# Performance work log

Measured on AMD Instinct MI355X. Metric: run time of the kernel, lower is better.

Reference implementation:

```python
import jax, jax.numpy as jnp
import numpy as np

EMBEDDING_DIM = 64
NUM_EMBEDDINGS = 512


def setup_inputs() -> dict:
    key = jax.random.key(0)
    k1, k2 = jax.random.split(key)
    inputs = jax.random.normal(k1, (64, 32, 32, EMBEDDING_DIM), dtype=jnp.float32)
    # codebook: (embedding_dim, num_embeddings), matching the Keras weight layout
    embeddings = jax.random.normal(k2, (EMBEDDING_DIM, NUM_EMBEDDINGS), dtype=jnp.float32)
    return {"inputs": inputs, "embeddings": embeddings}


def reference(inputs, embeddings):
    input_shape = inputs.shape
    flat = inputs.reshape(-1, EMBEDDING_DIM)  # [N, D]
    distances = (
        jnp.sum(flat * flat, axis=1, keepdims=True)
        + jnp.sum(embeddings * embeddings, axis=0, keepdims=True)
        - 2.0 * (flat @ embeddings)
    )  # [N, K]
    encoding_indices = jnp.argmin(distances, axis=1)  # [N]
    # one-hot @ embeddings.T == row gather from embeddings.T
    quantized = jnp.take(embeddings.T, encoding_indices, axis=0)  # [N, D]
    quantized = quantized.reshape(input_shape)
    return quantized, encoding_indices
```

## Files before the change

### kernel.cpp

```cpp
#include <hip/hip_runtime.h>

#define D 64
#define K 512
#define NT (K / 16)
#define TAU 0.01f

typedef float  f32x4  __attribute__((ext_vector_type(4)));
typedef short  bf16x8 __attribute__((ext_vector_type(8)));

__device__ inline unsigned short bf16_rne(float f) {
    union { float f; unsigned u; } v; v.f = f;
    unsigned r = v.u + 0x7FFFu + ((v.u >> 16) & 1u);
    return (unsigned short)(r >> 16);
}
__device__ inline float bf16_val(unsigned short b) {
    union { float f; unsigned u; } v; v.u = ((unsigned)b) << 16;
    return v.f;
}
__device__ inline void split8(const float* p, bf16x8& h, bf16x8& l) {
    float4 a = *(const float4*)p;
    float4 b = *(const float4*)(p + 4);
    float f[8] = {a.x, a.y, a.z, a.w, b.x, b.y, b.z, b.w};
#pragma unroll
    for (int j = 0; j < 8; ++j) {
        unsigned short hb = bf16_rne(f[j]);
        float lo = f[j] - bf16_val(hb);
        h[j] = (short)hb;
        l[j] = (short)bf16_rne(lo);
    }
}

__global__ void vq_prep(const float* __restrict__ emb,
                        float* __restrict__ embT,
                        float* __restrict__ enorm,
                        bf16x8* __restrict__ bhi,
                        bf16x8* __restrict__ blo) {
    int t = blockIdx.x * blockDim.x + threadIdx.x;
    int nt = t >> 7, c = (t >> 6) & 1, lane = t & 63;
    int k  = nt * 16 + (lane & 15);
    int d0 = c * 32 + ((lane >> 4) << 3);
    bf16x8 h, l;
#pragma unroll
    for (int j = 0; j < 8; ++j) {
        float xv = emb[(d0 + j) * K + k];
        unsigned short hb = bf16_rne(xv);
        float lo = xv - bf16_val(hb);
        h[j] = (short)hb;
        l[j] = (short)bf16_rne(lo);
    }
    int off = (nt * 2 + c) * 64 + lane;
    bhi[off] = h; blo[off] = l;

    if (t < K) {
        float s = 0.f;
#pragma unroll
        for (int d = 0; d < D; ++d) {
            float v = emb[d * K + t];
            embT[t * D + d] = v;
            s += v * v;
        }
        enorm[t] = s;
    }
}

__global__ __launch_bounds__(256, 2) void vq_mfma(
    const float* __restrict__ x,
    const float* __restrict__ embT,
    const float* __restrict__ enorm,
    const bf16x8* __restrict__ bhi,
    const bf16x8* __restrict__ blo,
    float* __restrict__ outq,
    float* __restrict__ outidx) {
    const int tid  = threadIdx.x;
    const int wave = __builtin_amdgcn_readfirstlane(tid >> 6);
    const int lane = tid & 63;
    const int col  = lane & 15;
    const int grp  = lane >> 4;
    const int rt0  = (blockIdx.x * 4 + wave) * 2;

    bf16x8 ah[2][2], al[2][2];
#pragma unroll
    for (int t = 0; t < 2; ++t) {
        const float* xr = x + (size_t)((rt0 + t) * 16 + col) * D + grp * 8;
        split8(xr,      ah[t][0], al[t][0]);
        split8(xr + 32, ah[t][1], al[t][1]);
    }

    float b1[2][4], b2[2][4];
    int   bi[2][4];
#pragma unroll
    for (int t = 0; t < 2; ++t)
#pragma unroll
        for (int q = 0; q < 4; ++q) {
            b1[t][q] = -3.4e38f; b2[t][q] = -3.4e38f; bi[t][q] = 0;
        }

#pragma unroll 2
    for (int nt = 0; nt < NT; ++nt) {
        int fo = (nt * 2) * 64 + lane;
        bf16x8 bh0 = bhi[fo], bh1 = bhi[fo + 64];
        bf16x8 bl0 = blo[fo], bl1 = blo[fo + 64];
        float env = enorm[nt * 16 + col] * -0.5f;
        f32x4 acc[2];
#pragma unroll
        for (int t = 0; t < 2; ++t) {
            acc[t] = f32x4{env, env, env, env};
            acc[t] = __builtin_amdgcn_mfma_f32_16x16x32_bf16(ah[t][0], bh0, acc[t], 0, 0, 0);
            acc[t] = __builtin_amdgcn_mfma_f32_16x16x32_bf16(ah[t][1], bh1, acc[t], 0, 0, 0);
            acc[t] = __builtin_amdgcn_mfma_f32_16x16x32_bf16(ah[t][0], bl0, acc[t], 0, 0, 0);
            acc[t] = __builtin_amdgcn_mfma_f32_16x16x32_bf16(ah[t][1], bl1, acc[t], 0, 0, 0);
            acc[t] = __builtin_amdgcn_mfma_f32_16x16x32_bf16(al[t][0], bh0, acc[t], 0, 0, 0);
            acc[t] = __builtin_amdgcn_mfma_f32_16x16x32_bf16(al[t][1], bh1, acc[t], 0, 0, 0);
        }
        int kk = nt * 16 + col;
#pragma unroll
        for (int t = 0; t < 2; ++t)
#pragma unroll
            for (int q = 0; q < 4; ++q) {
                float v = acc[t][q];
                bool gt = v > b1[t][q];
                b2[t][q] = gt ? b1[t][q] : fmaxf(b2[t][q], v);
                b1[t][q] = gt ? v : b1[t][q];
                bi[t][q] = gt ? kk : bi[t][q];
            }
    }

#pragma unroll
    for (int t = 0; t < 2; ++t)
#pragma unroll
        for (int q = 0; q < 4; ++q) {
            float v1 = b1[t][q], v2 = b2[t][q];
            int   i1 = bi[t][q];
#pragma unroll
            for (int m = 1; m <= 8; m <<= 1) {
                float o1 = __shfl_xor(v1, m);
                float o2 = __shfl_xor(v2, m);
                int   oi = __shfl_xor(i1, m);
                float nb2 = fmaxf(fminf(v1, o1), fmaxf(v2, o2));
                if (o1 > v1 || (o1 == v1 && oi < i1)) { v1 = o1; i1 = oi; }
                v2 = nb2;
            }
            b1[t][q] = v1; b2[t][q] = v2; bi[t][q] = i1;
        }

#pragma unroll
    for (int t = 0; t < 2; ++t)
#pragma unroll
        for (int q = 0; q < 4; ++q) {
            unsigned long long m = __ballot(b1[t][q] - b2[t][q] < TAU);
            if (m == 0ull) continue;
            for (int g = 0; g < 4; ++g) {
                if (!((m >> (g * 16)) & 1ull)) continue;
                int row = (rt0 + t) * 16 + g * 4 + q;
                const float4* x4 = (const float4*)(x + (size_t)row * D);
                float4 xr[16];
#pragma unroll
                for (int j = 0; j < 16; ++j) xr[j] = x4[j];
                float xn = 0.f;
#pragma unroll
                for (int j = 0; j < 16; ++j)
                    xn += xr[j].x * xr[j].x + xr[j].y * xr[j].y +
                          xr[j].z * xr[j].z + xr[j].w * xr[j].w;
                float best = 3.4e38f; int bb = 0;
#pragma unroll
                for (int kk = 0; kk < 8; ++kk) {
                    int k = lane * 8 + kk;
                    const float4* e4 = (const float4*)(embT + (size_t)k * D);
                    float d0 = 0.f, d1 = 0.f, d2 = 0.f, d3 = 0.f;
#pragma unroll
                    for (int j = 0; j < 4; ++j) {
                        float4 e0 = e4[j*4+0], e1 = e4[j*4+1];
                        float4 e2 = e4[j*4+2], e3 = e4[j*4+3];
                        d0 += xr[j*4+0].x*e0.x + xr[j*4+0].y*e0.y + xr[j*4+0].z*e0.z + xr[j*4+0].w*e0.w;
                        d1 += xr[j*4+1].x*e1.x + xr[j*4+1].y*e1.y + xr[j*4+1].z*e1.z + xr[j*4+1].w*e1.w;
                        d2 += xr[j*4+2].x*e2.x + xr[j*4+2].y*e2.y + xr[j*4+2].z*e2.z + xr[j*4+2].w*e2.w;
                        d3 += xr[j*4+3].x*e3.x + xr[j*4+3].y*e3.y + xr[j*4+3].z*e3.z + xr[j*4+3].w*e3.w;
                    }
                    float dist = (xn + enorm[k]) - 2.0f * ((d0 + d1) + (d2 + d3));
                    if (dist < best) { best = dist; bb = k; }
                }
#pragma unroll
                for (int mm = 1; mm <= 32; mm <<= 1) {
                    float od = __shfl_xor(best, mm);
                    int   oi = __shfl_xor(bb, mm);
                    if (od < best || (od == best && oi < bb)) { best = od; bb = oi; }
                }
                if (grp == g) bi[t][q] = bb;
            }
        }

#pragma unroll
    for (int t = 0; t < 2; ++t) {
        int rbase = (rt0 + t) * 16;
#pragma unroll
        for (int q = 0; q < 4; ++q) {
            if (col == q) {
                int row = rbase + grp * 4 + q;
                outidx[row] = (float)bi[t][q];
            }
        }
#pragma unroll
        for (int g = 0; g < 4; ++g)
#pragma unroll
            for (int q = 0; q < 4; ++q) {
                int kidx = __shfl(bi[t][q], g * 16);
                int row  = rbase + g * 4 + q;
                outq[(size_t)row * D + lane] = embT[(size_t)kidx * D + lane];
            }
    }
}

extern "C" void kernel_launch(void* const* d_in, const int* in_sizes, int n_in,
                              void* d_out, int out_size, void* d_ws, size_t ws_size,
                              hipStream_t stream) {
    const float* x   = (const float*)d_in[0];
    const float* emb = (const float*)d_in[1];
    int nrows = in_sizes[0] / D;

    char* w = (char*)d_ws;
    float*  embT   = (float*)w;   w += (size_t)K * D * 4;
    float*  enorm  = (float*)w;   w += (size_t)K * 4;
    bf16x8* bhi    = (bf16x8*)w;  w += (size_t)NT * 2 * 64 * 16;
    bf16x8* blo    = (bf16x8*)w;

    float* outq   = (float*)d_out;
    float* outidx = (float*)d_out + (size_t)nrows * D;

    vq_prep<<<16, 256, 0, stream>>>(emb, embT, enorm, bhi, blo);
    vq_mfma<<<nrows / 128, 256, 0, stream>>>(x, embT, enorm, bhi, blo,
                                             outq, outidx);
}
```

Measured before the change: 49.66 us.

## Split codebook across wave pairs, merge top-2 via LDS, vectorize gather

Each block now handles 64 rows, and each pair of waves splits the 512-entry codebook in half. Per-half best and second-best values are merged through shared memory, and the fallback exact recheck runs in one wave per pair. The three MFMA chains (hi*hi, hi*lo, lo*hi) now start from zero and run independently, so they can overlap instead of forming one serial dependency chain. The output gather becomes a coalesced float4 copy driven by indices staged in LDS. This doubles the grid size and raises the occupancy hint, at the cost of extra syncthreads and LDS traffic.

```diff
diff --git a/kernel.cpp b/kernel.cpp
--- a/kernel.cpp
+++ b/kernel.cpp
@@ -3,6 +3,7 @@
 #define D 64
 #define K 512
 #define NT (K / 16)
+#define HNT (NT / 2)
 #define TAU 0.01f
 
 typedef float  f32x4  __attribute__((ext_vector_type(4)));
@@ -63,7 +64,7 @@
     }
 }
 
-__global__ __launch_bounds__(256, 2) void vq_mfma(
+__global__ __launch_bounds__(256, 4) void vq_mfma(
     const float* __restrict__ x,
     const float* __restrict__ embT,
     const float* __restrict__ enorm,
@@ -76,7 +77,14 @@
     const int lane = tid & 63;
     const int col  = lane & 15;
     const int grp  = lane >> 4;
-    const int rt0  = (blockIdx.x * 4 + wave) * 2;
+    const int pair = wave >> 1;
+    const int half = wave & 1;
+    const int rowB = blockIdx.x * 64;
+    const int rt0  = (rowB >> 4) + pair * 2;
+
+    __shared__ float l1[2][64], l2[2][64];
+    __shared__ int   li[2][64];
+    __shared__ int   sfin[64];
 
     bf16x8 ah[2][2], al[2][2];
 #pragma unroll
@@ -95,34 +103,32 @@
             b1[t][q] = -3.4e38f; b2[t][q] = -3.4e38f; bi[t][q] = 0;
         }
 
+    const f32x4 zero4 = {0.f, 0.f, 0.f, 0.f};
 #pragma unroll 2
-    for (int nt = 0; nt < NT; ++nt) {
+    for (int it = 0; it < HNT; ++it) {
+        const int nt = half * HNT + it;
         int fo = (nt * 2) * 64 + lane;
         bf16x8 bh0 = bhi[fo], bh1 = bhi[fo + 64];
         bf16x8 bl0 = blo[fo], bl1 = blo[fo + 64];
-        float env = enorm[nt * 16 + col] * -0.5f;
-        f32x4 acc[2];
+        float env2 = enorm[nt * 16 + col] * -0.5f;
+        int kk = nt * 16 + col;
 #pragma unroll
         for (int t = 0; t < 2; ++t) {
-            acc[t] = f32x4{env, env, env, env};
-            acc[t] = __builtin_amdgcn_mfma_f32_16x16x32_bf16(ah[t][0], bh0, acc[t], 0, 0, 0);
-            acc[t] = __builtin_amdgcn_mfma_f32_16x16x32_bf16(ah[t][1], bh1, acc[t], 0, 0, 0);
-            acc[t] = __builtin_amdgcn_mfma_f32_16x16x32_bf16(ah[t][0], bl0, acc[t], 0, 0, 0);
-            acc[t] = __builtin_amdgcn_mfma_f32_16x16x32_bf16(ah[t][1], bl1, acc[t], 0, 0, 0);
-            acc[t] = __builtin_amdgcn_mfma_f32_16x16x32_bf16(al[t][0], bh0, acc[t], 0, 0, 0);
-            acc[t] = __builtin_amdgcn_mfma_f32_16x16x32_bf16(al[t][1], bh1, acc[t], 0, 0, 0);
-        }
-        int kk = nt * 16 + col;
-#pragma unroll
-        for (int t = 0; t < 2; ++t)
+            f32x4 hh = __builtin_amdgcn_mfma_f32_16x16x32_bf16(ah[t][0], bh0, zero4, 0, 0, 0);
+            f32x4 hl = __builtin_amdgcn_mfma_f32_16x16x32_bf16(ah[t][0], bl0, zero4, 0, 0, 0);
+            f32x4 lh = __builtin_amdgcn_mfma_f32_16x16x32_bf16(al[t][0], bh0, zero4, 0, 0, 0);
+            hh = __builtin_amdgcn_mfma_f32_16x16x32_bf16(ah[t][1], bh1, hh, 0, 0, 0);
+            hl = __builtin_amdgcn_mfma_f32_16x16x32_bf16(ah[t][1], bl1, hl, 0, 0, 0);
+            lh = __builtin_amdgcn_mfma_f32_16x16x32_bf16(al[t][1], bh1, lh, 0, 0, 0);
 #pragma unroll
             for (int q = 0; q < 4; ++q) {
-                float v = acc[t][q];
+                float v = (hh[q] + hl[q]) + (lh[q] + env2);
                 bool gt = v > b1[t][q];
-                b2[t][q] = gt ? b1[t][q] : fmaxf(b2[t][q], v);
+                b2[t][q] = fmaxf(b2[t][q], fminf(b1[t][q], v));
                 b1[t][q] = gt ? v : b1[t][q];
                 bi[t][q] = gt ? kk : bi[t][q];
             }
+        }
     }
 
 #pragma unroll
@@ -146,67 +152,88 @@
 #pragma unroll
     for (int t = 0; t < 2; ++t)
 #pragma unroll
-        for (int q = 0; q < 4; ++q) {
-            unsigned long long m = __ballot(b1[t][q] - b2[t][q] < TAU);
-            if (m == 0ull) continue;
-            for (int g = 0; g < 4; ++g) {
-                if (!((m >> (g * 16)) & 1ull)) continue;
-                int row = (rt0 + t) * 16 + g * 4 + q;
-                const float4* x4 = (const float4*)(x + (size_t)row * D);
-                float4 xr[16];
-#pragma unroll
-                for (int j = 0; j < 16; ++j) xr[j] = x4[j];
-                float xn = 0.f;
-#pragma unroll
-                for (int j = 0; j < 16; ++j)
-                    xn += xr[j].x * xr[j].x + xr[j].y * xr[j].y +
-                          xr[j].z * xr[j].z + xr[j].w * xr[j].w;
-                float best = 3.4e38f; int bb = 0;
+        for (int q = 0; q < 4; ++q)
+            if (col == q) {
+                int rib = pair * 32 + t * 16 + grp * 4 + q;
+                l1[half][rib] = b1[t][q];
+                l2[half][rib] = b2[t][q];
+                li[half][rib] = bi[t][q];
+            }
+    __syncthreads();
+
+    if (half == 0) {
+        int rib  = pair * 32 + (lane & 31);
+        float a1 = l1[0][rib], h1 = l1[1][rib];
+        float a2 = l2[0][rib], h2 = l2[1][rib];
+        int   ai = li[0][rib], hi = li[1][rib];
+        bool hw  = h1 > a1;
+        float fb1 = hw ? h1 : a1;
+        int   fbi = hw ? hi : ai;
+        float fb2 = fmaxf(fmaxf(a2, h2), fminf(a1, h1));
+        if (lane < 32) {
+            sfin[rib] = fbi;
+            outidx[rowB + rib] = (float)fbi;
+        }
+        unsigned long long mask =
+            __ballot((lane < 32) && (fb1 - fb2 < TAU));
+        while (mask) {
+            int bit = __ffsll((long long)mask) - 1;
+            mask &= mask - 1;
+            int ribf = pair * 32 + bit;
+            int row  = rowB + ribf;
+            const float4* x4 = (const float4*)(x + (size_t)row * D);
+            float xn = 0.f;
+            float dd[8];
+#pragma unroll
+            for (int kk = 0; kk < 8; ++kk) dd[kk] = 0.f;
+#pragma unroll
+            for (int c = 0; c < 4; ++c) {
+                float4 xc0 = x4[c*4+0], xc1 = x4[c*4+1];
+                float4 xc2 = x4[c*4+2], xc3 = x4[c*4+3];
+                xn += xc0.x*xc0.x + xc0.y*xc0.y + xc0.z*xc0.z + xc0.w*xc0.w
+                    + xc1.x*xc1.x + xc1.y*xc1.y + xc1.z*xc1.z + xc1.w*xc1.w
+                    + xc2.x*xc2.x + xc2.y*xc2.y + xc2.z*xc2.z + xc2.w*xc2.w
+                    + xc3.x*xc3.x + xc3.y*xc3.y + xc3.z*xc3.z + xc3.w*xc3.w;
 #pragma unroll
                 for (int kk = 0; kk < 8; ++kk) {
-                    int k = lane * 8 + kk;
-                    const float4* e4 = (const float4*)(embT + (size_t)k * D);
-                    float d0 = 0.f, d1 = 0.f, d2 = 0.f, d3 = 0.f;
-#pragma unroll
-                    for (int j = 0; j < 4; ++j) {
-                        float4 e0 = e4[j*4+0], e1 = e4[j*4+1];
-                        float4 e2 = e4[j*4+2], e3 = e4[j*4+3];
-                        d0 += xr[j*4+0].x*e0.x + xr[j*4+0].y*e0.y + xr[j*4+0].z*e0.z + xr[j*4+0].w*e0.w;
-                        d1 += xr[j*4+1].x*e1.x + xr[j*4+1].y*e1.y + xr[j*4+1].z*e1.z + xr[j*4+1].w*e1.w;
-                        d2 += xr[j*4+2].x*e2.x + xr[j*4+2].y*e2.y + xr[j*4+2].z*e2.z + xr[j*4+2].w*e2.w;
-                        d3 += xr[j*4+3].x*e3.x + xr[j*4+3].y*e3.y + xr[j*4+3].z*e3.z + xr[j*4+3].w*e3.w;
-                    }
-                    float dist = (xn + enorm[k]) - 2.0f * ((d0 + d1) + (d2 + d3));
-                    if (dist < best) { best = dist; bb = k; }
+                    const float4* e4 =
+                        (const float4*)(embT + (size_t)(lane * 8 + kk) * D) + c * 4;
+                    float4 e0 = e4[0], e1 = e4[1], e2 = e4[2], e3 = e4[3];
+                    dd[kk] += xc0.x*e0.x + xc0.y*e0.y + xc0.z*e0.z + xc0.w*e0.w
+                            + xc1.x*e1.x + xc1.y*e1.y + xc1.z*e1.z + xc1.w*e1.w
+                            + xc2.x*e2.x + xc2.y*e2.y + xc2.z*e2.z + xc2.w*e2.w
+                            + xc3.x*e3.x + xc3.y*e3.y + xc3.z*e3.z + xc3.w*e3.w;
                 }
-#pragma unroll
-                for (int mm = 1; mm <= 32; mm <<= 1) {
-                    float od = __shfl_xor(best, mm);
-                    int   oi = __shfl_xor(bb, mm);
-                    if (od < best || (od == best && oi < bb)) { best = od; bb = oi; }
-                }
-                if (grp == g) bi[t][q] = bb;
-            }
-        }
-
-#pragma unroll
-    for (int t = 0; t < 2; ++t) {
-        int rbase = (rt0 + t) * 16;
-#pragma unroll
-        for (int q = 0; q < 4; ++q) {
-            if (col == q) {
-                int row = rbase + grp * 4 + q;
-                outidx[row] = (float)bi[t][q];
-            }
-        }
-#pragma unroll
-        for (int g = 0; g < 4; ++g)
-#pragma unroll
-            for (int q = 0; q < 4; ++q) {
-                int kidx = __shfl(bi[t][q], g * 16);
-                int row  = rbase + g * 4 + q;
-                outq[(size_t)row * D + lane] = embT[(size_t)kidx * D + lane];
-            }
+            }
+            float best = 3.4e38f; int bb = 0;
+#pragma unroll
+            for (int kk = 0; kk < 8; ++kk) {
+                int k = lane * 8 + kk;
+                float dist = (xn + enorm[k]) - 2.0f * dd[kk];
+                if (dist < best) { best = dist; bb = k; }
+            }
+#pragma unroll
+            for (int mm = 1; mm <= 32; mm <<= 1) {
+                float od = __shfl_xor(best, mm);
+                int   oi = __shfl_xor(bb, mm);
+                if (od < best || (od == best && oi < bb)) { best = od; bb = oi; }
+            }
+            if (lane == 0) {
+                sfin[ribf] = bb;
+                outidx[row] = (float)bb;
+            }
+        }
+    }
+    __syncthreads();
+
+    const float4* ef4 = (const float4*)embT;
+    float4* oq4 = (float4*)(outq + (size_t)rowB * D);
+#pragma unroll
+    for (int i = 0; i < 4; ++i) {
+        int f  = tid + i * 256;
+        int rr = f >> 4;
+        int j  = f & 15;
+        oq4[f] = ef4[sfin[rr] * 16 + j];
     }
 }
 
@@ -227,6 +254,6 @@
     float* outidx = (float*)d_out + (size_t)nrows * D;
 
     vq_prep<<<16, 256, 0, stream>>>(emb, embT, enorm, bhi, blo);
-    vq_mfma<<<nrows / 128, 256, 0, stream>>>(x, embT, enorm, bhi, blo,
-                                             outq, outidx);
-}
+    vq_mfma<<<nrows / 64, 256, 0, stream>>>(x, embT, enorm, bhi, blo,
+                                            outq, outidx);
+}
```

After: 110.6 us. 2.23x slower.

## Stage codebook fragments through double-buffered LDS and split MFMA chains

Applied to the files above, without the earlier changes.

The codebook hi/lo bf16 fragments are now loaded cooperatively into a double-buffered shared-memory tile with a register prefetch two tiles ahead, replacing the per-wave global loads. The old single chain of six dependent MFMAs becomes three independent two-MFMA chains that are summed afterwards, shortening the dependency latency. The exact-recheck fallback is reordered to stream x in chunks rather than holding 16 float4 registers, which lowers register pressure. The cost is a __syncthreads every iteration and extra VALU adds per tile.

```diff
diff --git a/kernel.cpp b/kernel.cpp
--- a/kernel.cpp
+++ b/kernel.cpp
@@ -78,6 +78,8 @@
     const int grp  = lane >> 4;
     const int rt0  = (blockIdx.x * 4 + wave) * 2;
 
+    __shared__ bf16x8 sB[2][256];
+
     bf16x8 ah[2][2], al[2][2];
 #pragma unroll
     for (int t = 0; t < 2; ++t) {
@@ -95,34 +97,41 @@
             b1[t][q] = -3.4e38f; b2[t][q] = -3.4e38f; bi[t][q] = 0;
         }
 
-#pragma unroll 2
+    bf16x8 pf = (tid < 128) ? bhi[tid] : blo[tid - 128];
+    sB[0][tid] = pf;
+    pf = (tid < 128) ? bhi[128 + tid] : blo[tid];
+    __syncthreads();
+
+    const f32x4 zero4 = {0.f, 0.f, 0.f, 0.f};
     for (int nt = 0; nt < NT; ++nt) {
-        int fo = (nt * 2) * 64 + lane;
-        bf16x8 bh0 = bhi[fo], bh1 = bhi[fo + 64];
-        bf16x8 bl0 = blo[fo], bl1 = blo[fo + 64];
-        float env = enorm[nt * 16 + col] * -0.5f;
-        f32x4 acc[2];
+        const int cur = nt & 1;
+        if (nt + 1 < NT) sB[cur ^ 1][tid] = pf;
+        if (nt + 2 < NT)
+            pf = (tid < 128) ? bhi[(nt + 2) * 128 + tid]
+                             : blo[(nt + 2) * 128 + (tid - 128)];
+
+        bf16x8 bh0 = sB[cur][lane],       bh1 = sB[cur][64 + lane];
+        bf16x8 bl0 = sB[cur][128 + lane], bl1 = sB[cur][192 + lane];
+        float env2 = enorm[nt * 16 + col] * -0.5f;
+        int kk = nt * 16 + col;
 #pragma unroll
         for (int t = 0; t < 2; ++t) {
-            acc[t] = f32x4{env, env, env, env};
-            acc[t] = __builtin_amdgcn_mfma_f32_16x16x32_bf16(ah[t][0], bh0, acc[t], 0, 0, 0);
-            acc[t] = __builtin_amdgcn_mfma_f32_16x16x32_bf16(ah[t][1], bh1, acc[t], 0, 0, 0);
-            acc[t] = __builtin_amdgcn_mfma_f32_16x16x32_bf16(ah[t][0], bl0, acc[t], 0, 0, 0);
-            acc[t] = __builtin_amdgcn_mfma_f32_16x16x32_bf16(ah[t][1], bl1, acc[t], 0, 0, 0);
-            acc[t] = __builtin_amdgcn_mfma_f32_16x16x32_bf16(al[t][0], bh0, acc[t], 0, 0, 0);
-            acc[t] = __builtin_amdgcn_mfma_f32_16x16x32_bf16(al[t][1], bh1, acc[t], 0, 0, 0);
-        }
-        int kk = nt * 16 + col;
-#pragma unroll
-        for (int t = 0; t < 2; ++t)
+            f32x4 hh = __builtin_amdgcn_mfma_f32_16x16x32_bf16(ah[t][0], bh0, zero4, 0, 0, 0);
+            f32x4 hl = __builtin_amdgcn_mfma_f32_16x16x32_bf16(ah[t][0], bl0, zero4, 0, 0, 0);
+            f32x4 lh = __builtin_amdgcn_mfma_f32_16x16x32_bf16(al[t][0], bh0, zero4, 0, 0, 0);
+            hh = __builtin_amdgcn_mfma_f32_16x16x32_bf16(ah[t][1], bh1, hh, 0, 0, 0);
+            hl = __builtin_amdgcn_mfma_f32_16x16x32_bf16(ah[t][1], bl1, hl, 0, 0, 0);
+            lh = __builtin_amdgcn_mfma_f32_16x16x32_bf16(al[t][1], bh1, lh, 0, 0, 0);
 #pragma unroll
             for (int q = 0; q < 4; ++q) {
-                float v = acc[t][q];
+                float v = (hh[q] + hl[q]) + (lh[q] + env2);
                 bool gt = v > b1[t][q];
-                b2[t][q] = gt ? b1[t][q] : fmaxf(b2[t][q], v);
+                b2[t][q] = fmaxf(b2[t][q], fminf(b1[t][q], v));
                 b1[t][q] = gt ? v : b1[t][q];
                 bi[t][q] = gt ? kk : bi[t][q];
             }
+        }
+        __syncthreads();
     }
 
 #pragma unroll
@@ -153,30 +162,34 @@
                 if (!((m >> (g * 16)) & 1ull)) continue;
                 int row = (rt0 + t) * 16 + g * 4 + q;
                 const float4* x4 = (const float4*)(x + (size_t)row * D);
-                float4 xr[16];
-#pragma unroll
-                for (int j = 0; j < 16; ++j) xr[j] = x4[j];
                 float xn = 0.f;
-#pragma unroll
-                for (int j = 0; j < 16; ++j)
-                    xn += xr[j].x * xr[j].x + xr[j].y * xr[j].y +
-                          xr[j].z * xr[j].z + xr[j].w * xr[j].w;
+                float dd[8];
+#pragma unroll
+                for (int kk = 0; kk < 8; ++kk) dd[kk] = 0.f;
+#pragma unroll
+                for (int c = 0; c < 4; ++c) {
+                    float4 xc0 = x4[c*4+0], xc1 = x4[c*4+1];
+                    float4 xc2 = x4[c*4+2], xc3 = x4[c*4+3];
+                    xn += xc0.x*xc0.x + xc0.y*xc0.y + xc0.z*xc0.z + xc0.w*xc0.w
+                        + xc1.x*xc1.x + xc1.y*xc1.y + xc1.z*xc1.z + xc1.w*xc1.w
+                        + xc2.x*xc2.x + xc2.y*xc2.y + xc2.z*xc2.z + xc2.w*xc2.w
+                        + xc3.x*xc3.x + xc3.y*xc3.y + xc3.z*xc3.z + xc3.w*xc3.w;
+#pragma unroll
+                    for (int kk = 0; kk < 8; ++kk) {
+                        const float4* e4 =
+                            (const float4*)(embT + (size_t)(lane * 8 + kk) * D) + c * 4;
+                        float4 e0 = e4[0], e1 = e4[1], e2 = e4[2], e3 = e4[3];
+                        dd[kk] += xc0.x*e0.x + xc0.y*e0.y + xc0.z*e0.z + xc0.w*e0.w
+                                + xc1.x*e1.x + xc1.y*e1.y + xc1.z*e1.z + xc1.w*e1.w
+                                + xc2.x*e2.x + xc2.y*e2.y + xc2.z*e2.z + xc2.w*e2.w
+                                + xc3.x*e3.x + xc3.y*e3.y + xc3.z*e3.z + xc3.w*e3.w;
+                    }
+                }
                 float best = 3.4e38f; int bb = 0;
 #pragma unroll
                 for (int kk = 0; kk < 8; ++kk) {
                     int k = lane * 8 + kk;
-                    const float4* e4 = (const float4*)(embT + (size_t)k * D);
-                    float d0 = 0.f, d1 = 0.f, d2 = 0.f, d3 = 0.f;
-#pragma unroll
-                    for (int j = 0; j < 4; ++j) {
-                        float4 e0 = e4[j*4+0], e1 = e4[j*4+1];
-                        float4 e2 = e4[j*4+2], e3 = e4[j*4+3];
-                        d0 += xr[j*4+0].x*e0.x + xr[j*4+0].y*e0.y + xr[j*4+0].z*e0.z + xr[j*4+0].w*e0.w;
-                        d1 += xr[j*4+1].x*e1.x + xr[j*4+1].y*e1.y + xr[j*4+1].z*e1.z + xr[j*4+1].w*e1.w;
-                        d2 += xr[j*4+2].x*e2.x + xr[j*4+2].y*e2.y + xr[j*4+2].z*e2.z + xr[j*4+2].w*e2.w;
-                        d3 += xr[j*4+3].x*e3.x + xr[j*4+3].y*e3.y + xr[j*4+3].z*e3.z + xr[j*4+3].w*e3.w;
-                    }
-                    float dist = (xn + enorm[k]) - 2.0f * ((d0 + d1) + (d2 + d3));
+                    float dist = (xn + enorm[k]) - 2.0f * dd[kk];
                     if (dist < best) { best = dist; bb = k; }
                 }
 #pragma unroll
```

Result: slower. 68.93 us (+38.8%).

## Prefetch next codebook tile and split MFMA chains into independent accumulators

Applied to the files above, without the earlier changes.

Software-pipelines the codebook fragment and norm loads by fetching tile nt+1 while tile nt is computed. It also breaks each serial six-MFMA dependency chain into three independent two-MFMA chains (hi*hi, hi*lo, lo*hi) that are summed afterwards, cutting MFMA dependency stalls. The second-best update is rewritten branch-free with fmin/fmax. The cost is more accumulator registers and a slightly different floating-point summation order, which the tolerance-based refinement path absorbs.

```diff
diff --git a/kernel.cpp b/kernel.cpp
--- a/kernel.cpp
+++ b/kernel.cpp
@@ -95,34 +95,38 @@
             b1[t][q] = -3.4e38f; b2[t][q] = -3.4e38f; bi[t][q] = 0;
         }
 
-#pragma unroll 2
+    bf16x8 nh0 = bhi[lane], nh1 = bhi[64 + lane];
+    bf16x8 nl0 = blo[lane], nl1 = blo[64 + lane];
+    float  nen = enorm[col];
+
+    const f32x4 zero4 = {0.f, 0.f, 0.f, 0.f};
     for (int nt = 0; nt < NT; ++nt) {
-        int fo = (nt * 2) * 64 + lane;
-        bf16x8 bh0 = bhi[fo], bh1 = bhi[fo + 64];
-        bf16x8 bl0 = blo[fo], bl1 = blo[fo + 64];
-        float env = enorm[nt * 16 + col] * -0.5f;
-        f32x4 acc[2];
+        bf16x8 bh0 = nh0, bh1 = nh1, bl0 = nl0, bl1 = nl1;
+        float env2 = nen * -0.5f;
+        int kk = nt * 16 + col;
+        if (nt + 1 < NT) {
+            int fo = (nt + 1) * 128 + lane;
+            nh0 = bhi[fo]; nh1 = bhi[fo + 64];
+            nl0 = blo[fo]; nl1 = blo[fo + 64];
+            nen = enorm[(nt + 1) * 16 + col];
+        }
 #pragma unroll
         for (int t = 0; t < 2; ++t) {
-            acc[t] = f32x4{env, env, env, env};
-            acc[t] = __builtin_amdgcn_mfma_f32_16x16x32_bf16(ah[t][0], bh0, acc[t], 0, 0, 0);
-            acc[t] = __builtin_amdgcn_mfma_f32_16x16x32_bf16(ah[t][1], bh1, acc[t], 0, 0, 0);
-            acc[t] = __builtin_amdgcn_mfma_f32_16x16x32_bf16(ah[t][0], bl0, acc[t], 0, 0, 0);
-            acc[t] = __builtin_amdgcn_mfma_f32_16x16x32_bf16(ah[t][1], bl1, acc[t], 0, 0, 0);
-            acc[t] = __builtin_amdgcn_mfma_f32_16x16x32_bf16(al[t][0], bh0, acc[t], 0, 0, 0);
-            acc[t] = __builtin_amdgcn_mfma_f32_16x16x32_bf16(al[t][1], bh1, acc[t], 0, 0, 0);
-        }
-        int kk = nt * 16 + col;
-#pragma unroll
-        for (int t = 0; t < 2; ++t)
+            f32x4 hh = __builtin_amdgcn_mfma_f32_16x16x32_bf16(ah[t][0], bh0, zero4, 0, 0, 0);
+            f32x4 hl = __builtin_amdgcn_mfma_f32_16x16x32_bf16(ah[t][0], bl0, zero4, 0, 0, 0);
+            f32x4 lh = __builtin_amdgcn_mfma_f32_16x16x32_bf16(al[t][0], bh0, zero4, 0, 0, 0);
+            hh = __builtin_amdgcn_mfma_f32_16x16x32_bf16(ah[t][1], bh1, hh, 0, 0, 0);
+            hl = __builtin_amdgcn_mfma_f32_16x16x32_bf16(ah[t][1], bl1, hl, 0, 0, 0);
+            lh = __builtin_amdgcn_mfma_f32_16x16x32_bf16(al[t][1], bh1, lh, 0, 0, 0);
 #pragma unroll
             for (int q = 0; q < 4; ++q) {
-                float v = acc[t][q];
+                float v = (hh[q] + hl[q]) + (lh[q] + env2);
                 bool gt = v > b1[t][q];
-                b2[t][q] = gt ? b1[t][q] : fmaxf(b2[t][q], v);
+                b2[t][q] = fmaxf(b2[t][q], fminf(b1[t][q], v));
                 b1[t][q] = gt ? v : b1[t][q];
                 bi[t][q] = gt ? kk : bi[t][q];
             }
+        }
     }
 
 #pragma unroll
```

Measured after the change: 47.40 us. 1.05x faster.
